# Performance work log

Hardware: AMD Instinct MI355X
Metric: run time of the kernel (lower is better)

The kernel has to match this reference:

```python
import jax, jax.numpy as jnp
import numpy as np

N = 100000      # num_nodes
E = 1600000     # num_edges (avg degree 16)
EMB = 128       # emb_dim
HID = 128       # hidden_size
REPR = 64       # repr_dim


def setup_inputs() -> dict:
    key = jax.random.key(0)
    k0, k1, k2, k3 = jax.random.split(key, 4)
    edge_index = jax.random.randint(k0, (2, E), 0, N)
    node_emb = jax.random.normal(k1, (N, EMB), jnp.float32) * 0.1
    # GCNConv weights: glorot-like init, bias zeros (PyG default)
    W1 = jax.random.normal(k2, (EMB, HID), jnp.float32) * (1.0 / np.sqrt(EMB))
    b1 = jnp.zeros((HID,), jnp.float32)
    W2 = jax.random.normal(k3, (HID, REPR), jnp.float32) * (1.0 / np.sqrt(HID))
    b2 = jnp.zeros((REPR,), jnp.float32)
    return {"edge_index": edge_index, "node_emb": node_emb,
            "W1": W1, "b1": b1, "W2": W2, "b2": b2}


def reference(edge_index, node_emb, W1, b1, W2, b2):
    # PyG GCNConv: add self-loops, symmetric degree normalization,
    # out = scatter_add(norm * (x W)[src] -> dst) + b
    loops = jnp.arange(N, dtype=edge_index.dtype)
    src = jnp.concatenate([edge_index[0], loops])  # [E+N]
    dst = jnp.concatenate([edge_index[1], loops])
    deg = jax.ops.segment_sum(jnp.ones_like(src, dtype=node_emb.dtype), dst,
                              num_segments=N)
    dinv = jax.lax.rsqrt(deg)  # deg >= 1 thanks to self-loops
    norm = dinv[src] * dinv[dst]  # [E+N]

    def gcn_conv(x, W, b):
        h = x @ W                                   # [N, out]
        msg = norm[:, None] * h[src]                # gather + scale, [E+N, out]
        return jax.ops.segment_sum(msg, dst, num_segments=N) + b

    x = jax.nn.relu(gcn_conv(node_emb, W1, b1))
    # F.dropout(training=False) is identity in eval mode
    return gcn_conv(x, W2, b2)
```

## Files before the change

kernel.cpp:

```cpp
#include <hip/hip_runtime.h>
#include <hip/hip_bf16.h>
#include <stdint.h>


static constexpr int KD = 128;
static constexpr int BSH = 10;
static constexpr int MAXB = 256;
static constexpr int CHUNK = 8192;
static constexpr int CAP = 24576;

typedef short bf16x8 __attribute__((ext_vector_type(8)));
typedef float f32x4  __attribute__((ext_vector_type(4)));

__device__ __forceinline__ unsigned short f2bf(float f) {
    __hip_bfloat16 b = __float2bfloat16(f);
    return *reinterpret_cast<unsigned short*>(&b);
}
__device__ __forceinline__ float bflo(unsigned v) { return __uint_as_float(v << 16); }
__device__ __forceinline__ float bfhi(unsigned v) { return __uint_as_float(v & 0xffff0000u); }

__global__ __launch_bounds__(256) void init_misc(const float* __restrict__ W1,
        const float* __restrict__ W2, unsigned short* __restrict__ Wt1,
        unsigned short* __restrict__ Wt2, int* __restrict__ bcur, int nbuck) {
    int t = blockIdx.x * 256 + threadIdx.x;
    if (t < 128 * 128) {
        int k = t >> 7, nn = t & 127;
        Wt1[nn * 128 + k] = f2bf(W1[t]);
    } else if (t < 128 * 128 + 128 * 64) {
        int i = t - 128 * 128;
        int k = i >> 6, nn = i & 63;
        Wt2[nn * 128 + k] = f2bf(W2[i]);
    } else if (t < 128 * 128 + 128 * 64 + MAXB) {
        int b = t - (128 * 128 + 128 * 64);
        bcur[b] = b * CAP;
    }
}

__global__ __launch_bounds__(256) void multisplit(const int* __restrict__ src,
        const int* __restrict__ dst, int* __restrict__ bcur,
        int* __restrict__ packed, int e, int nbuck) {
    __shared__ int cnt[MAXB], lbase[MAXB], wbase[MAXB], vcnt[MAXB], scanbuf[256];
    __shared__ int buf[CHUNK];
    const int t = threadIdx.x;
    const int e0 = blockIdx.x * CHUNK;
    const int m = min(CHUNK, e - e0);

    for (int i = t; i < nbuck; i += 256) cnt[i] = 0;
    __syncthreads();
    for (int i = t; i < m; i += 256) atomicAdd(&cnt[dst[e0 + i] >> BSH], 1);
    __syncthreads();
    int v = (t < nbuck) ? cnt[t] : 0;
    scanbuf[t] = v;
    __syncthreads();
    for (int off = 1; off < 256; off <<= 1) {
        int u = (t >= off) ? scanbuf[t - off] : 0;
        __syncthreads();
        scanbuf[t] += u;
        __syncthreads();
    }
    int excl = scanbuf[t] - v;
    if (t < nbuck) {
        lbase[t] = excl;
        vcnt[t] = v;
        wbase[t] = v ? atomicAdd(&bcur[t], v) : 0;
        cnt[t] = excl;
    }
    __syncthreads();
    for (int i = t; i < m; i += 256) {
        int d = dst[e0 + i], s = src[e0 + i];
        int b = d >> BSH;
        int p = atomicAdd(&cnt[b], 1);
        buf[p] = ((d & ((1 << BSH) - 1)) << 22) | s;
    }
    __syncthreads();
    int wv = t >> 6, ln = t & 63;
    for (int b = wv; b < nbuck; b += 4) {
        int c = vcnt[b], st = lbase[b], g = wbase[b];
        int end = min(c, (b + 1) * CAP - g);
        for (int i = ln; i < end; i += 64) packed[g + i] = buf[st + i];
    }
}

__global__ __launch_bounds__(256) void bucket_build(const int* __restrict__ packed,
        const int* __restrict__ bcur, int* __restrict__ roff, int* __restrict__ degN,
        float* __restrict__ dinv, int* __restrict__ csr, int n) {
    __shared__ int deg[1 << BSH];
    __shared__ int cur[1 << BSH];
    __shared__ int wsum[4];
    const int t = threadIdx.x;
    const int b = blockIdx.x;
    const int nodeBase = b << BSH;
    const int nn = min(1 << BSH, n - nodeBase);
    const int e0 = b * CAP, e1 = bcur[b];

    for (int i = t; i < (1 << BSH); i += 256) deg[i] = 0;
    __syncthreads();
    for (int i = e0 + t; i < e1; i += 256)
        atomicAdd(&deg[(unsigned)packed[i] >> 22], 1);
    __syncthreads();

    const int i0 = t * 4;
    int d0 = deg[i0], d1 = deg[i0 + 1], d2 = deg[i0 + 2], d3 = deg[i0 + 3];
    int tsum = d0 + d1 + d2 + d3;
    int lane = t & 63, wv = t >> 6;
    int v = tsum;
    for (int off = 1; off < 64; off <<= 1) {
        int u = __shfl_up(v, off, 64);
        if (lane >= off) v += u;
    }
    if (lane == 63) wsum[wv] = v;
    __syncthreads();
    int woff = 0;
    for (int i = 0; i < wv; ++i) woff += wsum[i];
    int excl = v - tsum + woff;
    int p0 = excl, p1 = excl + d0, p2 = p1 + d1, p3 = p2 + d2;
    cur[i0] = p0; cur[i0 + 1] = p1; cur[i0 + 2] = p2; cur[i0 + 3] = p3;
#pragma unroll
    for (int j = 0; j < 4; ++j) {
        int li = i0 + j;
        if (li < nn) {
            int pp = (j == 0) ? p0 : (j == 1) ? p1 : (j == 2) ? p2 : p3;
            int dd = (j == 0) ? d0 : (j == 1) ? d1 : (j == 2) ? d2 : d3;
            roff[nodeBase + li] = e0 + pp;
            degN[nodeBase + li] = dd;
            dinv[nodeBase + li] = rsqrtf((float)(dd + 1));
        }
    }
    __syncthreads();

    for (int i = e0 + t; i < e1; i += 256) {
        unsigned pk = (unsigned)packed[i];
        int dl = pk >> 22;
        int s = pk & 0x3FFFFF;
        int slot = atomicAdd(&cur[dl], 1);
        csr[e0 + slot] = s;
    }
}

template<int C, bool XBF>
__global__ __launch_bounds__(256) void gemm_mfma(const void* __restrict__ xv,
        const unsigned short* __restrict__ Wt, const float* __restrict__ dinv,
        unsigned short* __restrict__ out, int n)
{
    constexpr int KP = KD + 8;
    constexpr int WP = 64 + 8;
    __shared__ __align__(16) unsigned short xt[64 * KP];
    __shared__ __align__(16) unsigned short lw[C * WP];
    const int t = threadIdx.x;
    const int w = t >> 6, lane = t & 63;
    const int quad = lane >> 4, l16 = lane & 15;
    const int row0 = blockIdx.x * 64;

    for (int i = t; i < 64 * 32; i += 256) {
        int r = i >> 5, c4 = (i & 31) * 4;
        int row = row0 + r;
        ushort4 pk = make_ushort4(0, 0, 0, 0);
        if (row < n) {
            if constexpr (XBF) {
                pk = *reinterpret_cast<const ushort4*>(
                    &((const unsigned short*)xv)[(size_t)row * KD + c4]);
            } else {
                float4 v = *reinterpret_cast<const float4*>(
                    &((const float*)xv)[(size_t)row * KD + c4]);
                pk.x = f2bf(v.x); pk.y = f2bf(v.y); pk.z = f2bf(v.z); pk.w = f2bf(v.w);
            }
        }
        *reinterpret_cast<ushort4*>(&xt[r * KP + c4]) = pk;
    }

    f32x4 acc[C / 16];
#pragma unroll
    for (int i = 0; i < C / 16; ++i) acc[i] = (f32x4)(0.f);

    for (int h = 0; h < 2; ++h) {
        __syncthreads();
        for (int i = t; i < C * 16; i += 256) {
            int nr = i >> 4, j = (i & 15) * 4;
            *reinterpret_cast<ushort4*>(&lw[nr * WP + j]) =
                *reinterpret_cast<const ushort4*>(&Wt[nr * KD + h * 64 + j]);
        }
        __syncthreads();
#pragma unroll
        for (int kt = 0; kt < 2; ++kt) {
            bf16x8 af = *reinterpret_cast<const bf16x8*>(
                &xt[(w * 16 + l16) * KP + h * 64 + kt * 32 + quad * 8]);
#pragma unroll
            for (int ct = 0; ct < C / 16; ++ct) {
                bf16x8 bfr = *reinterpret_cast<const bf16x8*>(
                    &lw[(ct * 16 + l16) * WP + kt * 32 + quad * 8]);
                acc[ct] = __builtin_amdgcn_mfma_f32_16x16x32_bf16(af, bfr, acc[ct], 0, 0, 0);
            }
        }
    }

#pragma unroll
    for (int j = 0; j < 4; ++j) {
        int row = row0 + w * 16 + quad * 4 + j;
        if (row < n) {
            float s = dinv[row];
#pragma unroll
            for (int ct = 0; ct < C / 16; ++ct)
                out[(size_t)row * C + ct * 16 + l16] = f2bf(acc[ct][j] * s);
        }
    }
}

__global__ __launch_bounds__(256) void gather128(const unsigned* __restrict__ h32,
        const int* __restrict__ roff, const int* __restrict__ degN,
        const int* __restrict__ csr, const float* __restrict__ dinv,
        const float* __restrict__ b, unsigned* __restrict__ out, int n)
{
    int wid = (blockIdx.x * 256 + threadIdx.x) >> 6;
    int lane = threadIdx.x & 63;
    if (wid >= n) return;
    const unsigned* hl = h32 + lane;
    unsigned sv = hl[(size_t)wid * 64];
    float ax = bflo(sv), ay = bfhi(sv);
    float bx = 0.f, by = 0.f;
    int e0 = roff[wid], e1 = e0 + degN[wid];
    for (int base = e0; base < e1; base += 64) {
        int m = e1 - base; if (m > 64) m = 64;
        int idx = (lane < m) ? csr[base + lane] : 0;
        int j = 0;
        for (; j + 8 <= m; j += 8) {
            int u0 = __shfl(idx, j+0), u1 = __shfl(idx, j+1);
            int u2 = __shfl(idx, j+2), u3 = __shfl(idx, j+3);
            int u4 = __shfl(idx, j+4), u5 = __shfl(idx, j+5);
            int u6 = __shfl(idx, j+6), u7 = __shfl(idx, j+7);
            unsigned v0 = hl[(size_t)u0 * 64];
            unsigned v1 = hl[(size_t)u1 * 64];
            unsigned v2 = hl[(size_t)u2 * 64];
            unsigned v3 = hl[(size_t)u3 * 64];
            unsigned v4 = hl[(size_t)u4 * 64];
            unsigned v5 = hl[(size_t)u5 * 64];
            unsigned v6 = hl[(size_t)u6 * 64];
            unsigned v7 = hl[(size_t)u7 * 64];
            ax += bflo(v0) + bflo(v1); ay += bfhi(v0) + bfhi(v1);
            bx += bflo(v2) + bflo(v3); by += bfhi(v2) + bfhi(v3);
            ax += bflo(v4) + bflo(v5); ay += bfhi(v4) + bfhi(v5);
            bx += bflo(v6) + bflo(v7); by += bfhi(v6) + bfhi(v7);
        }
        for (; j < m; ++j) {
            int u = __shfl(idx, j);
            unsigned v = hl[(size_t)u * 64];
            ax += bflo(v); ay += bfhi(v);
        }
    }
    ax += bx; ay += by;
    float s = dinv[wid];
    float2 bb = ((const float2*)b)[lane];
    ax = fmaxf(s * ax + bb.x, 0.f);
    ay = fmaxf(s * ay + bb.y, 0.f);
    out[(size_t)wid * 64 + lane] = (unsigned)f2bf(ax) | ((unsigned)f2bf(ay) << 16);
}

__global__ __launch_bounds__(256) void gather64(const unsigned* __restrict__ h32,
        const int* __restrict__ roff, const int* __restrict__ degN,
        const int* __restrict__ csr, const float* __restrict__ dinv,
        const float* __restrict__ b, float* __restrict__ out, int n)
{
    int wid = (blockIdx.x * 256 + threadIdx.x) >> 6;
    int lane = threadIdx.x & 63;
    if (wid >= n) return;
    const int half = lane >> 5, cp = lane & 31;
    const unsigned* hl = h32 + cp;
    float ax = 0.f, ay = 0.f, bx = 0.f, by = 0.f;
    int e0 = roff[wid], e1 = e0 + degN[wid];
    for (int base = e0; base < e1; base += 64) {
        int m = e1 - base; if (m > 64) m = 64;
        int idx = (lane < m) ? csr[base + lane] : 0;
        int j = 0;
        for (; j + 8 <= m; j += 8) {
            int u0 = __shfl(idx, j + 0 + half);
            int u1 = __shfl(idx, j + 2 + half);
            int u2 = __shfl(idx, j + 4 + half);
            int u3 = __shfl(idx, j + 6 + half);
            unsigned v0 = hl[(size_t)u0 * 32];
            unsigned v1 = hl[(size_t)u1 * 32];
            unsigned v2 = hl[(size_t)u2 * 32];
            unsigned v3 = hl[(size_t)u3 * 32];
            ax += bflo(v0) + bflo(v1); ay += bfhi(v0) + bfhi(v1);
            bx += bflo(v2) + bflo(v3); by += bfhi(v2) + bfhi(v3);
        }
        for (; j + 2 <= m; j += 2) {
            int u = __shfl(idx, j + half);
            unsigned v = hl[(size_t)u * 32];
            ax += bflo(v); ay += bfhi(v);
        }
        if (j < m) {
            int u = __shfl(idx, j);
            if (half == 0) {
                unsigned v = hl[(size_t)u * 32];
                ax += bflo(v); ay += bfhi(v);
            }
        }
    }
    ax += bx; ay += by;
    ax += __shfl_xor(ax, 32, 64);
    ay += __shfl_xor(ay, 32, 64);
    unsigned sv = hl[(size_t)wid * 32];
    ax += bflo(sv); ay += bfhi(sv);
    if (half == 0) {
        float s = dinv[wid];
        float2 bb = ((const float2*)b)[cp];
        ((float2*)out)[(size_t)wid * 32 + cp] =
            make_float2(s * ax + bb.x, s * ay + bb.y);
    }
}

extern "C" void kernel_launch(void* const* d_in, const int* in_sizes, int n_in,
                              void* d_out, int out_size, void* d_ws, size_t ws_size,
                              hipStream_t stream)
{
    const int* ei = (const int*)d_in[0];
    const int E = in_sizes[0] / 2;
    const float* emb = (const float*)d_in[1];
    const int N = in_sizes[1] / KD;
    const float* W1 = (const float*)d_in[2];
    const float* b1 = (const float*)d_in[3];
    const float* W2 = (const float*)d_in[4];
    const float* b2 = (const float*)d_in[5];
    const int* src = ei;
    const int* dst = ei + E;
    const int nbuck = (N + (1 << BSH) - 1) >> BSH;

    char* p = (char*)d_ws;
    auto alloc = [&](size_t bytes) { char* q = p; p += (bytes + 255) & ~(size_t)255; return q; };
    unsigned short* h1 = (unsigned short*)alloc((size_t)N * 128 * sizeof(unsigned short));
    unsigned short* x2 = (unsigned short*)alloc((size_t)N * 128 * sizeof(unsigned short));
    int*   csr    = (int*)  alloc((size_t)nbuck * CAP * sizeof(int));
    int*   packed = (int*)  alloc((size_t)nbuck * CAP * sizeof(int));
    int*   roff   = (int*)  alloc((size_t)N * sizeof(int));
    int*   degN   = (int*)  alloc((size_t)N * sizeof(int));
    float* dinv   = (float*)alloc((size_t)N * sizeof(float));
    int*   bcur   = (int*)  alloc(MAXB * sizeof(int));
    unsigned short* Wt1 = (unsigned short*)alloc(128 * 128 * sizeof(unsigned short));
    unsigned short* Wt2 = (unsigned short*)alloc(64 * 128 * sizeof(unsigned short));
    unsigned short* h2 = h1;

    init_misc<<<97, 256, 0, stream>>>(W1, W2, Wt1, Wt2, bcur, nbuck);
    multisplit<<<(E + CHUNK - 1) / CHUNK, 256, 0, stream>>>(src, dst, bcur, packed, E, nbuck);
    bucket_build<<<nbuck, 256, 0, stream>>>(packed, bcur, roff, degN, dinv, csr, N);

    gemm_mfma<128, false><<<(N + 63) / 64, 256, 0, stream>>>(emb, Wt1, dinv, h1, N);
    gather128<<<(N + 3) / 4, 256, 0, stream>>>((const unsigned*)h1, roff, degN, csr,
                                               dinv, b1, (unsigned*)x2, N);

    gemm_mfma<64, true><<<(N + 63) / 64, 256, 0, stream>>>(x2, Wt2, dinv, h2, N);
    gather64<<<(N + 3) / 4, 256, 0, stream>>>((const unsigned*)h2, roff, degN, csr,
                                              dinv, b2, (float*)d_out, N);
}
```

Before: 322.5 us.

## Vectorize neighbor gathers to 16-byte loads and halve bucket size

The two aggregation kernels now have each lane load a uint4 (8 bf16 features) per neighbor instead of 4 bytes. One wavefront therefore processes 4 neighbors (128-wide layer) or 8 neighbors (64-wide layer) at once, and the partial sums are combined with cross-lane shuffle reductions at the end. The goal is fewer load instructions and more memory requests in flight during the irregular gathers. The CSR build buckets shrink from 1024 to 512 nodes with half the capacity, which doubles the block count in bucket_build for better GPU occupancy. The cost is more shuffle reduction work and less headroom per bucket before it overflows.

```diff
diff --git a/kernel.cpp b/kernel.cpp
--- a/kernel.cpp
+++ b/kernel.cpp
@@ -4,10 +4,10 @@
 
 
 static constexpr int KD = 128;
-static constexpr int BSH = 10;
+static constexpr int BSH = 9;
 static constexpr int MAXB = 256;
 static constexpr int CHUNK = 8192;
-static constexpr int CAP = 24576;
+static constexpr int CAP = 12288;
 
 typedef short bf16x8 __attribute__((ext_vector_type(8)));
 typedef float f32x4  __attribute__((ext_vector_type(4)));
@@ -18,6 +18,15 @@
 }
 __device__ __forceinline__ float bflo(unsigned v) { return __uint_as_float(v << 16); }
 __device__ __forceinline__ float bfhi(unsigned v) { return __uint_as_float(v & 0xffff0000u); }
+__device__ __forceinline__ unsigned pk2(float lo, float hi) {
+    return (unsigned)f2bf(lo) | ((unsigned)f2bf(hi) << 16);
+}
+__device__ __forceinline__ void acc8(float* a, uint4 v) {
+    a[0] += bflo(v.x); a[1] += bfhi(v.x);
+    a[2] += bflo(v.y); a[3] += bfhi(v.y);
+    a[4] += bflo(v.z); a[5] += bfhi(v.z);
+    a[6] += bflo(v.w); a[7] += bfhi(v.w);
+}
 
 __global__ __launch_bounds__(256) void init_misc(const float* __restrict__ W1,
         const float* __restrict__ W2, unsigned short* __restrict__ Wt1,
@@ -99,9 +108,9 @@
         atomicAdd(&deg[(unsigned)packed[i] >> 22], 1);
     __syncthreads();
 
-    const int i0 = t * 4;
-    int d0 = deg[i0], d1 = deg[i0 + 1], d2 = deg[i0 + 2], d3 = deg[i0 + 3];
-    int tsum = d0 + d1 + d2 + d3;
+    const int i0 = t * 2;
+    int d0 = deg[i0], d1 = deg[i0 + 1];
+    int tsum = d0 + d1;
     int lane = t & 63, wv = t >> 6;
     int v = tsum;
     for (int off = 1; off < 64; off <<= 1) {
@@ -113,18 +122,17 @@
     int woff = 0;
     for (int i = 0; i < wv; ++i) woff += wsum[i];
     int excl = v - tsum + woff;
-    int p0 = excl, p1 = excl + d0, p2 = p1 + d1, p3 = p2 + d2;
-    cur[i0] = p0; cur[i0 + 1] = p1; cur[i0 + 2] = p2; cur[i0 + 3] = p3;
-#pragma unroll
-    for (int j = 0; j < 4; ++j) {
-        int li = i0 + j;
-        if (li < nn) {
-            int pp = (j == 0) ? p0 : (j == 1) ? p1 : (j == 2) ? p2 : p3;
-            int dd = (j == 0) ? d0 : (j == 1) ? d1 : (j == 2) ? d2 : d3;
-            roff[nodeBase + li] = e0 + pp;
-            degN[nodeBase + li] = dd;
-            dinv[nodeBase + li] = rsqrtf((float)(dd + 1));
-        }
+    int p0 = excl, p1 = excl + d0;
+    cur[i0] = p0; cur[i0 + 1] = p1;
+    if (i0 < nn) {
+        roff[nodeBase + i0] = e0 + p0;
+        degN[nodeBase + i0] = d0;
+        dinv[nodeBase + i0] = rsqrtf((float)(d0 + 1));
+    }
+    if (i0 + 1 < nn) {
+        roff[nodeBase + i0 + 1] = e0 + p1;
+        degN[nodeBase + i0 + 1] = d1;
+        dinv[nodeBase + i0 + 1] = rsqrtf((float)(d1 + 1));
     }
     __syncthreads();
 
@@ -205,106 +213,127 @@
     }
 }
 
-__global__ __launch_bounds__(256) void gather128(const unsigned* __restrict__ h32,
+__global__ __launch_bounds__(256) void gather128(const uint4* __restrict__ H,
         const int* __restrict__ roff, const int* __restrict__ degN,
         const int* __restrict__ csr, const float* __restrict__ dinv,
-        const float* __restrict__ b, unsigned* __restrict__ out, int n)
+        const float* __restrict__ b, uint4* __restrict__ out, int n)
 {
     int wid = (blockIdx.x * 256 + threadIdx.x) >> 6;
     int lane = threadIdx.x & 63;
     if (wid >= n) return;
-    const unsigned* hl = h32 + lane;
-    unsigned sv = hl[(size_t)wid * 64];
-    float ax = bflo(sv), ay = bfhi(sv);
-    float bx = 0.f, by = 0.f;
+    const int qw = lane >> 4, cp = lane & 15;
+    const uint4* hl = H + cp;
+    float a[8] = {0.f, 0.f, 0.f, 0.f, 0.f, 0.f, 0.f, 0.f};
+    float c[8] = {0.f, 0.f, 0.f, 0.f, 0.f, 0.f, 0.f, 0.f};
     int e0 = roff[wid], e1 = e0 + degN[wid];
     for (int base = e0; base < e1; base += 64) {
         int m = e1 - base; if (m > 64) m = 64;
         int idx = (lane < m) ? csr[base + lane] : 0;
         int j = 0;
         for (; j + 8 <= m; j += 8) {
-            int u0 = __shfl(idx, j+0), u1 = __shfl(idx, j+1);
-            int u2 = __shfl(idx, j+2), u3 = __shfl(idx, j+3);
-            int u4 = __shfl(idx, j+4), u5 = __shfl(idx, j+5);
-            int u6 = __shfl(idx, j+6), u7 = __shfl(idx, j+7);
-            unsigned v0 = hl[(size_t)u0 * 64];
-            unsigned v1 = hl[(size_t)u1 * 64];
-            unsigned v2 = hl[(size_t)u2 * 64];
-            unsigned v3 = hl[(size_t)u3 * 64];
-            unsigned v4 = hl[(size_t)u4 * 64];
-            unsigned v5 = hl[(size_t)u5 * 64];
-            unsigned v6 = hl[(size_t)u6 * 64];
-            unsigned v7 = hl[(size_t)u7 * 64];
-            ax += bflo(v0) + bflo(v1); ay += bfhi(v0) + bfhi(v1);
-            bx += bflo(v2) + bflo(v3); by += bfhi(v2) + bfhi(v3);
-            ax += bflo(v4) + bflo(v5); ay += bfhi(v4) + bfhi(v5);
-            bx += bflo(v6) + bflo(v7); by += bfhi(v6) + bfhi(v7);
-        }
-        for (; j < m; ++j) {
-            int u = __shfl(idx, j);
-            unsigned v = hl[(size_t)u * 64];
-            ax += bflo(v); ay += bfhi(v);
-        }
-    }
-    ax += bx; ay += by;
-    float s = dinv[wid];
-    float2 bb = ((const float2*)b)[lane];
-    ax = fmaxf(s * ax + bb.x, 0.f);
-    ay = fmaxf(s * ay + bb.y, 0.f);
-    out[(size_t)wid * 64 + lane] = (unsigned)f2bf(ax) | ((unsigned)f2bf(ay) << 16);
-}
-
-__global__ __launch_bounds__(256) void gather64(const unsigned* __restrict__ h32,
+            int u0 = __shfl(idx, j + qw);
+            int u1 = __shfl(idx, j + 4 + qw);
+            uint4 v0 = hl[(size_t)u0 * 16];
+            uint4 v1 = hl[(size_t)u1 * 16];
+            acc8(a, v0);
+            acc8(c, v1);
+        }
+        for (; j + 4 <= m; j += 4) {
+            int u = __shfl(idx, j + qw);
+            uint4 v = hl[(size_t)u * 16];
+            acc8(a, v);
+        }
+        int r = m - j;
+        if (r) {
+            int u = __shfl(idx, min(j + qw, m - 1));
+            if (qw < r) {
+                uint4 v = hl[(size_t)u * 16];
+                acc8(a, v);
+            }
+        }
+    }
+#pragma unroll
+    for (int i = 0; i < 8; ++i) a[i] += c[i];
+#pragma unroll
+    for (int i = 0; i < 8; ++i) {
+        a[i] += __shfl_xor(a[i], 16, 64);
+        a[i] += __shfl_xor(a[i], 32, 64);
+    }
+    if (qw == 0) {
+        uint4 sv = hl[(size_t)wid * 16];
+        acc8(a, sv);
+        float s = dinv[wid];
+        float4 b0 = ((const float4*)b)[cp * 2];
+        float4 b1 = ((const float4*)b)[cp * 2 + 1];
+        float r0 = fmaxf(s * a[0] + b0.x, 0.f), r1 = fmaxf(s * a[1] + b0.y, 0.f);
+        float r2 = fmaxf(s * a[2] + b0.z, 0.f), r3 = fmaxf(s * a[3] + b0.w, 0.f);
+        float r4 = fmaxf(s * a[4] + b1.x, 0.f), r5 = fmaxf(s * a[5] + b1.y, 0.f);
+        float r6 = fmaxf(s * a[6] + b1.z, 0.f), r7 = fmaxf(s * a[7] + b1.w, 0.f);
+        uint4 o;
+        o.x = pk2(r0, r1); o.y = pk2(r2, r3); o.z = pk2(r4, r5); o.w = pk2(r6, r7);
+        out[(size_t)wid * 16 + cp] = o;
+    }
+}
+
+__global__ __launch_bounds__(256) void gather64(const uint4* __restrict__ H,
         const int* __restrict__ roff, const int* __restrict__ degN,
         const int* __restrict__ csr, const float* __restrict__ dinv,
-        const float* __restrict__ b, float* __restrict__ out, int n)
+        const float* __restrict__ b, float4* __restrict__ out, int n)
 {
     int wid = (blockIdx.x * 256 + threadIdx.x) >> 6;
     int lane = threadIdx.x & 63;
     if (wid >= n) return;
-    const int half = lane >> 5, cp = lane & 31;
-    const unsigned* hl = h32 + cp;
-    float ax = 0.f, ay = 0.f, bx = 0.f, by = 0.f;
+    const int oc = lane >> 3, cp = lane & 7;
+    const uint4* hl = H + cp;
+    float a[8] = {0.f, 0.f, 0.f, 0.f, 0.f, 0.f, 0.f, 0.f};
+    float c[8] = {0.f, 0.f, 0.f, 0.f, 0.f, 0.f, 0.f, 0.f};
     int e0 = roff[wid], e1 = e0 + degN[wid];
     for (int base = e0; base < e1; base += 64) {
         int m = e1 - base; if (m > 64) m = 64;
         int idx = (lane < m) ? csr[base + lane] : 0;
         int j = 0;
+        for (; j + 16 <= m; j += 16) {
+            int u0 = __shfl(idx, j + oc);
+            int u1 = __shfl(idx, j + 8 + oc);
+            uint4 v0 = hl[(size_t)u0 * 8];
+            uint4 v1 = hl[(size_t)u1 * 8];
+            acc8(a, v0);
+            acc8(c, v1);
+        }
         for (; j + 8 <= m; j += 8) {
-            int u0 = __shfl(idx, j + 0 + half);
-            int u1 = __shfl(idx, j + 2 + half);
-            int u2 = __shfl(idx, j + 4 + half);
-            int u3 = __shfl(idx, j + 6 + half);
-            unsigned v0 = hl[(size_t)u0 * 32];
-            unsigned v1 = hl[(size_t)u1 * 32];
-            unsigned v2 = hl[(size_t)u2 * 32];
-            unsigned v3 = hl[(size_t)u3 * 32];
-            ax += bflo(v0) + bflo(v1); ay += bfhi(v0) + bfhi(v1);
-            bx += bflo(v2) + bflo(v3); by += bfhi(v2) + bfhi(v3);
-        }
-        for (; j + 2 <= m; j += 2) {
-            int u = __shfl(idx, j + half);
-            unsigned v = hl[(size_t)u * 32];
-            ax += bflo(v); ay += bfhi(v);
-        }
-        if (j < m) {
-            int u = __shfl(idx, j);
-            if (half == 0) {
-                unsigned v = hl[(size_t)u * 32];
-                ax += bflo(v); ay += bfhi(v);
+            int u = __shfl(idx, j + oc);
+            uint4 v = hl[(size_t)u * 8];
+            acc8(a, v);
+        }
+        int r = m - j;
+        if (r) {
+            int u = __shfl(idx, min(j + oc, m - 1));
+            if (oc < r) {
+                uint4 v = hl[(size_t)u * 8];
+                acc8(a, v);
             }
         }
     }
-    ax += bx; ay += by;
-    ax += __shfl_xor(ax, 32, 64);
-    ay += __shfl_xor(ay, 32, 64);
-    unsigned sv = hl[(size_t)wid * 32];
-    ax += bflo(sv); ay += bfhi(sv);
-    if (half == 0) {
+#pragma unroll
+    for (int i = 0; i < 8; ++i) a[i] += c[i];
+#pragma unroll
+    for (int i = 0; i < 8; ++i) {
+        a[i] += __shfl_xor(a[i], 8, 64);
+        a[i] += __shfl_xor(a[i], 16, 64);
+        a[i] += __shfl_xor(a[i], 32, 64);
+    }
+    if (oc == 0) {
+        uint4 sv = hl[(size_t)wid * 8];
+        acc8(a, sv);
         float s = dinv[wid];
-        float2 bb = ((const float2*)b)[cp];
-        ((float2*)out)[(size_t)wid * 32 + cp] =
-            make_float2(s * ax + bb.x, s * ay + bb.y);
+        float4 b0 = ((const float4*)b)[cp * 2];
+        float4 b1 = ((const float4*)b)[cp * 2 + 1];
+        float4 o0 = make_float4(s * a[0] + b0.x, s * a[1] + b0.y,
+                                s * a[2] + b0.z, s * a[3] + b0.w);
+        float4 o1 = make_float4(s * a[4] + b1.x, s * a[5] + b1.y,
+                                s * a[6] + b1.z, s * a[7] + b1.w);
+        out[(size_t)wid * 16 + cp * 2] = o0;
+        out[(size_t)wid * 16 + cp * 2 + 1] = o1;
     }
 }
 
@@ -343,10 +372,10 @@
     bucket_build<<<nbuck, 256, 0, stream>>>(packed, bcur, roff, degN, dinv, csr, N);
 
     gemm_mfma<128, false><<<(N + 63) / 64, 256, 0, stream>>>(emb, Wt1, dinv, h1, N);
-    gather128<<<(N + 3) / 4, 256, 0, stream>>>((const unsigned*)h1, roff, degN, csr,
-                                               dinv, b1, (unsigned*)x2, N);
+    gather128<<<(N + 3) / 4, 256, 0, stream>>>((const uint4*)h1, roff, degN, csr,
+                                               dinv, b1, (uint4*)x2, N);
 
     gemm_mfma<64, true><<<(N + 63) / 64, 256, 0, stream>>>(x2, Wt2, dinv, h2, N);
-    gather64<<<(N + 3) / 4, 256, 0, stream>>>((const unsigned*)h2, roff, degN, csr,
-                                              dinv, b2, (float*)d_out, N);
-}
+    gather64<<<(N + 3) / 4, 256, 0, stream>>>((const uint4*)h2, roff, degN, csr,
+                                              dinv, b2, (float4*)d_out, N);
+}
```

Result: faster. 301.3 us (-6.6%).
